# Optimization experiments

Measured on AMD Instinct MI355X. Metric: run time of the kernel, lower is better.

The kernel has to match this reference:

```python
import jax, jax.numpy as jnp
import numpy as np

DIN = 4096
DOUT = 12288
NUM_GATES = DOUT // 3
OFFSET = 1
BS = 4096
Z = 1.0

# fixed 3x5 combine matrix from the module
M = jnp.array([[1., 0., 0., 0., 0.],
               [0., 0., 1., 1., -1.],
               [0., 1., 0., -1., 1.]], dtype=jnp.float32)


def _make_connections():
    g = np.arange(NUM_GATES, dtype=np.int64)
    starts = (g * 3 + OFFSET) % DIN
    conn = (starts[:, None] + np.arange(3, dtype=np.int64)[None, :]) % DIN
    return jnp.asarray(conn, dtype=jnp.int32)


def setup_inputs() -> dict:
    key = jax.random.key(0)
    kx, kw = jax.random.split(key)
    x = jax.random.normal(kx, (BS, DIN), dtype=jnp.float32)
    wgts = jax.random.normal(kw, (NUM_GATES, 3, 4), dtype=jnp.float32)
    connections = _make_connections()
    return {"x": x, "wgts": wgts, "connections": connections}


def reference(x, wgts, connections):
    bs = x.shape[0]
    # gather 3 inputs per gate: [bs, G, 3]
    gathered = x[:, connections]
    # append constant z -> [bs, G, 4]
    zcol = jnp.full((bs, NUM_GATES, 1), Z, dtype=x.dtype)
    inp = jnp.concatenate([gathered, zcol], axis=-1)
    # softmax-weighted small matmul (training path): [G,3,4] x [bs,G,4] -> [bs,G,3]
    wp = jax.nn.softmax(wgts, axis=-1)
    s = jnp.einsum('gik,bgk->bgi', wp, inp)
    # elementwise products -> [bs, G, 5]
    v4 = s[..., 0] * s[..., 1]
    v5 = s[..., 0] * s[..., 2]
    feats = jnp.concatenate([s, v4[..., None], v5[..., None]], axis=-1)
    # fixed 3x5 combine: [bs, G, 3]
    signals = jnp.einsum('rk,bgk->bgr', M, feats)
    # strided slice ::3 on last dim (size 3) keeps only index 0 -> [bs, G]
    out = signals[:, :, ::3].reshape(bs, -1)
    return out
```

## Files before the change

kernel.cpp:

```cpp
#include <hip/hip_runtime.h>

#define DIN 4096
#define NG  4096
#define BS  4096
#define RPB 8
#define BT  1024

typedef float v4f __attribute__((ext_vector_type(4)));

#define WAITVM(N) __builtin_amdgcn_s_waitcnt((N) | 0x0F70)

__device__ __forceinline__ void dma16(const float* g, float* lds) {
    __builtin_amdgcn_global_load_lds(
        (const __attribute__((address_space(1))) void*)g,
        (__attribute__((address_space(3))) void*)lds, 16, 0, 0);
}

__global__ __launch_bounds__(BT, 8) void fredkin_s0_dma(
    const float* __restrict__ x,
    const float* __restrict__ wgts,
    float* __restrict__ out)
{
    __shared__ float B0[DIN], B1[DIN], B2[DIN], B3[DIN];

    const int tid = threadIdx.x;
    const int w   = tid >> 6;
    const int l   = tid & 63;
    const int g0  = 4 * tid;

    float4 wq[4];
#pragma unroll
    for (int j = 0; j < 4; ++j) {
        float4 r = *reinterpret_cast<const float4*>(wgts + (size_t)(g0 + j) * 12);
        float m  = fmaxf(fmaxf(r.x, r.y), fmaxf(r.z, r.w));
        float e0 = __expf(r.x - m);
        float e1 = __expf(r.y - m);
        float e2 = __expf(r.z - m);
        float e3 = __expf(r.w - m);
        float inv = 1.0f / (e0 + e1 + e2 + e3);
        wq[j] = make_float4(e0 * inv, e1 * inv, e2 * inv, e3 * inv);
    }

    const int brow = blockIdx.x * RPB;
    const float* xb   = x   + (size_t)brow * DIN;
    float*       orow = out + (size_t)brow * NG + g0;
    const int doff = 256 * w + 4 * l;

    const int lb = (12 * tid) & (DIN - 1);
    const int i1 = (lb + 4)  & (DIN - 1);
    const int i2 = (lb + 8)  & (DIN - 1);
    const int i3 = (lb + 12) & (DIN - 1);

    dma16(xb + 0 * DIN + doff, B0 + 256 * w);
    dma16(xb + 1 * DIN + doff, B1 + 256 * w);
    dma16(xb + 2 * DIN + doff, B2 + 256 * w);

#define FRED_ITER(R, NWAIT, RBUF, WBUF, DO_DMA)                                     \
    {                                                                               \
        asm volatile("" ::: "memory");                                              \
        WAITVM(NWAIT);                                      \
        __builtin_amdgcn_s_barrier();             \
        asm volatile("" ::: "memory");                                              \
        if (DO_DMA) dma16(xb + (size_t)(R + 3) * DIN + doff, WBUF + 256 * w);       \
        float4 f0 = *reinterpret_cast<const float4*>(&RBUF[lb]);       \
        float4 f1 = *reinterpret_cast<const float4*>(&RBUF[i1]);       \
        float4 f2 = *reinterpret_cast<const float4*>(&RBUF[i2]);       \
        float e12 = __shfl_down(f0.x, 1);             \
        if (l == 63) e12 = RBUF[i3];              \
        v4f o;                                                                      \
        o.x = fmaf(wq[0].x, f0.y, fmaf(wq[0].y, f0.z, fmaf(wq[0].z, f0.w, wq[0].w))); \
        o.y = fmaf(wq[1].x, f1.x, fmaf(wq[1].y, f1.y, fmaf(wq[1].z, f1.z, wq[1].w))); \
        o.z = fmaf(wq[2].x, f1.w, fmaf(wq[2].y, f2.x, fmaf(wq[2].z, f2.y, wq[2].w))); \
        o.w = fmaf(wq[3].x, f2.z, fmaf(wq[3].y, f2.w, fmaf(wq[3].z, e12, wq[3].w))); \
        __builtin_nontemporal_store(o, reinterpret_cast<v4f*>(orow + (size_t)(R) * NG)); \
    }

    FRED_ITER(0, 2, B0, B3, 1)
    FRED_ITER(1, 3, B1, B0, 1)
    FRED_ITER(2, 4, B2, B1, 1)
    FRED_ITER(3, 5, B3, B2, 1)
    FRED_ITER(4, 5, B0, B3, 1)
    FRED_ITER(5, 5, B1, B0, 0)
    FRED_ITER(6, 4, B2, B1, 0)
    FRED_ITER(7, 3, B3, B2, 0)
#undef FRED_ITER
}

extern "C" void kernel_launch(void* const* d_in, const int* in_sizes, int n_in,
                              void* d_out, int out_size, void* d_ws, size_t ws_size,
                              hipStream_t stream) {
    const float* x    = (const float*)d_in[0];
    const float* wgts = (const float*)d_in[1];
    float* out = (float*)d_out;

    fredkin_s0_dma<<<dim3(BS / RPB), dim3(BT), 0, stream>>>(x, wgts, out);
}
```

Before: 116.3 us.

## Replace LDS DMA pipeline with direct global vector loads per row

Result: slower. 127.2 us (+9.4%).

```diff
diff --git a/kernel.cpp b/kernel.cpp
--- a/kernel.cpp
+++ b/kernel.cpp
@@ -8,23 +8,12 @@
 
 typedef float v4f __attribute__((ext_vector_type(4)));
 
-#define WAITVM(N) __builtin_amdgcn_s_waitcnt((N) | 0x0F70)
-
-__device__ __forceinline__ void dma16(const float* g, float* lds) {
-    __builtin_amdgcn_global_load_lds(
-        (const __attribute__((address_space(1))) void*)g,
-        (__attribute__((address_space(3))) void*)lds, 16, 0, 0);
-}
-
-__global__ __launch_bounds__(BT, 8) void fredkin_s0_dma(
+__global__ __launch_bounds__(BT, 4) void fredkin_s0_stream(
     const float* __restrict__ x,
     const float* __restrict__ wgts,
     float* __restrict__ out)
 {
-    __shared__ float B0[DIN], B1[DIN], B2[DIN], B3[DIN];
-
     const int tid = threadIdx.x;
-    const int w   = tid >> 6;
     const int l   = tid & 63;
     const int g0  = 4 * tid;
 
@@ -44,46 +33,27 @@
     const int brow = blockIdx.x * RPB;
     const float* xb   = x   + (size_t)brow * DIN;
     float*       orow = out + (size_t)brow * NG + g0;
-    const int doff = 256 * w + 4 * l;
 
     const int lb = (12 * tid) & (DIN - 1);
     const int i1 = (lb + 4)  & (DIN - 1);
     const int i2 = (lb + 8)  & (DIN - 1);
     const int i3 = (lb + 12) & (DIN - 1);
 
-    dma16(xb + 0 * DIN + doff, B0 + 256 * w);
-    dma16(xb + 1 * DIN + doff, B1 + 256 * w);
-    dma16(xb + 2 * DIN + doff, B2 + 256 * w);
-
-#define FRED_ITER(R, NWAIT, RBUF, WBUF, DO_DMA)                                     \
-    {                                                                               \
-        asm volatile("" ::: "memory");                                              \
-        WAITVM(NWAIT);                                      \
-        __builtin_amdgcn_s_barrier();             \
-        asm volatile("" ::: "memory");                                              \
-        if (DO_DMA) dma16(xb + (size_t)(R + 3) * DIN + doff, WBUF + 256 * w);       \
-        float4 f0 = *reinterpret_cast<const float4*>(&RBUF[lb]);       \
-        float4 f1 = *reinterpret_cast<const float4*>(&RBUF[i1]);       \
-        float4 f2 = *reinterpret_cast<const float4*>(&RBUF[i2]);       \
-        float e12 = __shfl_down(f0.x, 1);             \
-        if (l == 63) e12 = RBUF[i3];              \
-        v4f o;                                                                      \
-        o.x = fmaf(wq[0].x, f0.y, fmaf(wq[0].y, f0.z, fmaf(wq[0].z, f0.w, wq[0].w))); \
-        o.y = fmaf(wq[1].x, f1.x, fmaf(wq[1].y, f1.y, fmaf(wq[1].z, f1.z, wq[1].w))); \
-        o.z = fmaf(wq[2].x, f1.w, fmaf(wq[2].y, f2.x, fmaf(wq[2].z, f2.y, wq[2].w))); \
-        o.w = fmaf(wq[3].x, f2.z, fmaf(wq[3].y, f2.w, fmaf(wq[3].z, e12, wq[3].w))); \
-        __builtin_nontemporal_store(o, reinterpret_cast<v4f*>(orow + (size_t)(R) * NG)); \
+#pragma unroll
+    for (int r = 0; r < RPB; ++r) {
+        const float* xr = xb + (size_t)r * DIN;
+        float4 f0 = *reinterpret_cast<const float4*>(xr + lb);
+        float4 f1 = *reinterpret_cast<const float4*>(xr + i1);
+        float4 f2 = *reinterpret_cast<const float4*>(xr + i2);
+        float e12 = __shfl_down(f0.x, 1);
+        if (l == 63) e12 = xr[i3];
+        v4f o;
+        o.x = fmaf(wq[0].x, f0.y, fmaf(wq[0].y, f0.z, fmaf(wq[0].z, f0.w, wq[0].w)));
+        o.y = fmaf(wq[1].x, f1.x, fmaf(wq[1].y, f1.y, fmaf(wq[1].z, f1.z, wq[1].w)));
+        o.z = fmaf(wq[2].x, f1.w, fmaf(wq[2].y, f2.x, fmaf(wq[2].z, f2.y, wq[2].w)));
+        o.w = fmaf(wq[3].x, f2.z, fmaf(wq[3].y, f2.w, fmaf(wq[3].z, e12, wq[3].w)));
+        __builtin_nontemporal_store(o, reinterpret_cast<v4f*>(orow + (size_t)r * NG));
     }
-
-    FRED_ITER(0, 2, B0, B3, 1)
-    FRED_ITER(1, 3, B1, B0, 1)
-    FRED_ITER(2, 4, B2, B1, 1)
-    FRED_ITER(3, 5, B3, B2, 1)
-    FRED_ITER(4, 5, B0, B3, 1)
-    FRED_ITER(5, 5, B1, B0, 0)
-    FRED_ITER(6, 4, B2, B1, 0)
-    FRED_ITER(7, 3, B3, B2, 0)
-#undef FRED_ITER
 }
 
 extern "C" void kernel_launch(void* const* d_in, const int* in_sizes, int n_in,
@@ -93,5 +63,5 @@
     const float* wgts = (const float*)d_in[1];
     float* out = (float*)d_out;
 
-    fredkin_s0_dma<<<dim3(BS / RPB), dim3(BT), 0, stream>>>(x, wgts, out);
+    fredkin_s0_stream<<<dim3(BS / RPB), dim3(BT), 0, stream>>>(x, wgts, out);
 }
```
